# Kernel tuning notes

Measured on AMD Instinct MI355X. Metric: run time of the kernel, lower is better.

Reference implementation:

```python
import jax, jax.numpy as jnp
import numpy as np

EMB = 768

def setup_inputs() -> dict:
    key = jax.random.key(0)
    ks = jax.random.split(key, 9)
    B, N, E = 8, 2048, EMB
    s = 1.0 / np.sqrt(E)
    return {
        "x":  jax.random.normal(ks[0], (B, N, E), jnp.float32),
        "Wq": jax.random.normal(ks[1], (E, E), jnp.float32) * s,
        "bq": jnp.zeros((E,), jnp.float32),
        "Wk": jax.random.normal(ks[2], (E, E), jnp.float32) * s,
        "bk": jnp.zeros((E,), jnp.float32),
        "Wv": jax.random.normal(ks[3], (E, E), jnp.float32) * s,
        "bv": jnp.zeros((E,), jnp.float32),
        "Wo": jax.random.normal(ks[4], (E, E), jnp.float32) * s,
        "bo": jnp.zeros((E,), jnp.float32),
    }

def reference(x, Wq, bq, Wk, bk, Wv, bv, Wo, bo):
    # Single-head attention; scale uses full emb dim (as in the source).
    E = x.shape[-1]
    q = jnp.einsum('bne,ef->bnf', x, Wq) + bq
    k = jnp.einsum('bne,ef->bnf', x, Wk) + bk
    v = jnp.einsum('bne,ef->bnf', x, Wv) + bv
    scores = jnp.einsum('bqe,bke->bqk', q, k) / jnp.sqrt(jnp.asarray(E, x.dtype))
    attn = jax.nn.softmax(scores, axis=-1)  # dropout is identity in eval mode
    out = jnp.einsum('bqk,bke->bqe', attn, v)
    return jnp.einsum('bne,ef->bnf', out, Wo) + bo
```

## Files before the change

### kernel.cpp

```cpp
#include <hip/hip_runtime.h>
#include <hip/hip_fp16.h>
#include <stdint.h>

typedef unsigned short u16;
typedef __attribute__((ext_vector_type(8))) __bf16 bf16x8;
typedef __attribute__((ext_vector_type(4))) float f32x4;

#define SEQ 2048
#define EMB 768
#define NB  8
#define LDQK (2 * EMB)

#define VMCNT(n) asm volatile("s_waitcnt vmcnt(" #n ")" ::: "memory")
#define LGKM(n)                                            \
  do {                                                     \
    asm volatile("s_waitcnt lgkmcnt(" #n ")" ::: "memory"); \
    __builtin_amdgcn_sched_barrier(0);                     \
  } while (0)

__device__ __forceinline__ u16 f2bf(float f) {
  union { float f; uint32_t u; } a; a.f = f;
  uint32_t r = a.u + 0x7fffu + ((a.u >> 16) & 1u);
  return (u16)(r >> 16);
}
__device__ __forceinline__ float bf2f(u16 h) {
  union { uint32_t u; float f; } a; a.u = ((uint32_t)h) << 16;
  return a.f;
}

__device__ __forceinline__ void swz_bid(int& bx, int& by, int& bz)
{
  const int gx = gridDim.x, gy = gridDim.y;
  const int nwg = gx * gy * gridDim.z;
  const int lid = ((int)blockIdx.z * gy + (int)blockIdx.y) * gx +
                  (int)blockIdx.x;
  const int cpx = nwg >> 3;
  const int orig = (lid & 7) * cpx + (lid >> 3);
  bx = orig % gx;
  const int t = orig / gx;
  by = t % gy;
  bz = t / gy;
}

__global__ __launch_bounds__(256) void k_detect_bias(
    const u16* __restrict__ x, int* __restrict__ flag,
    const void* __restrict__ b0, const void* __restrict__ b1,
    const void* __restrict__ b2, const void* __restrict__ b3,
    float* __restrict__ biasf)
{
  const int tid = threadIdx.x;
  int bad = 0;
#pragma unroll
  for (int i = 0; i < 4; ++i) {
    const u16 h = x[(tid * 4 + i) * 2];
    const int e = (h >> 7) & 0xFF;
    bad += (e >= 160 && e <= 254) ? 1 : 0;
  }
#pragma unroll
  for (int off = 32; off > 0; off >>= 1) bad += __shfl_down(bad, off);
  __shared__ int cnt[4];
  __shared__ int sflag;
  if ((tid & 63) == 0) cnt[tid >> 6] = bad;
  __syncthreads();
  if (tid == 0) {
    const int f = (cnt[0] + cnt[1] + cnt[2] + cnt[3] > 200) ? 1 : 0;
    sflag = f;
    *flag = f;
  }
  __syncthreads();
  const int f32 = sflag;
#pragma unroll
  for (int z = 0; z < 4; ++z) {
    const void* src = (z == 0) ? b0 : (z == 1) ? b1 : (z == 2) ? b2 : b3;
#pragma unroll
    for (int i = 0; i < 3; ++i) {
      const int j = tid + i * 256;
      biasf[z * EMB + j] = f32 ? ((const float*)src)[j]
                               : bf2f(((const u16*)src)[j]);
    }
  }
}

__global__ __launch_bounds__(256) void k_convert_x(
    const void* __restrict__ src, u16* __restrict__ dst,
    const int* __restrict__ flag, int n4)
{
  const int i = blockIdx.x * 256 + threadIdx.x;
  if (i >= n4) return;
  if (*flag) {
    const float4 f = ((const float4*)src)[i];
    ushort4 o;
    o.x = f2bf(f.x); o.y = f2bf(f.y); o.z = f2bf(f.z); o.w = f2bf(f.w);
    ((ushort4*)dst)[i] = o;
  } else {
    ((ushort4*)dst)[i] = ((const ushort4*)src)[i];
  }
}

__global__ __launch_bounds__(256) void k_transpose_w(
    const void* __restrict__ W0, const void* __restrict__ W1,
    const void* __restrict__ W2, const void* __restrict__ W3,
    u16* __restrict__ WT, const int* __restrict__ flag)
{
  __shared__ u16 t[32][33];
  const int z = blockIdx.z;
  const void* in = (z == 0) ? W0 : (z == 1) ? W1 : (z == 2) ? W2 : W3;
  u16* out = WT + (size_t)z * EMB * EMB;
  const int c0 = blockIdx.x * 32, r0 = blockIdx.y * 32;
  const int tx = threadIdx.x, ty = threadIdx.y;
  const int f32 = *flag;
#pragma unroll
  for (int i = 0; i < 4; ++i) {
    const size_t idx = (size_t)(r0 + ty + i * 8) * EMB + c0 + tx;
    t[ty + i * 8][tx] = f32 ? f2bf(((const float*)in)[idx])
                            : ((const u16*)in)[idx];
  }
  __syncthreads();
#pragma unroll
  for (int i = 0; i < 4; ++i)
    out[(size_t)(c0 + ty + i * 8) * EMB + r0 + tx] = t[tx][ty + i * 8];
}

template <int EPI, int MFR, int NFR>
__device__ __forceinline__ void gemm_core256(
    const u16* __restrict__ A, int lda,
    const u16* __restrict__ BT, int ldbt,
    void* __restrict__ Cp, int ldc,
    const float* __restrict__ biasf, const int* __restrict__ of32,
    float scale, int K, int m0, int n0)
{
  constexpr int AQ = MFR * 1024;
  constexpr int BQ = NFR * 2048;
  constexpr int STRIDE = 2 * AQ + 2 * BQ;
  __shared__ __align__(16) u16 LDSU[2 * STRIDE];
  const int tid  = threadIdx.x;
  const int lane = tid & 63;
  const int wave = tid >> 6;
  const int wm   = wave >> 2;
  const int wn   = wave & 3;
  const int lrow = lane & 15;
  const int quad = lane >> 4;
  const int NT   = K >> 6;

  auto STAGEA = [&](int t, int kh) {
    constexpr int NCH = MFR * 128;
    const int buf = t & 1;
#pragma unroll
    for (int i = 0; i < 2; ++i) {
      const int c = i * 512 + tid;
      if (NCH == 1024 || c < NCH) {
        const int row = c >> 2;
        const int ss4 = (c & 3) ^ ((row >> 1) & 3);
        const u16* g = A + (size_t)(m0 + row) * lda + t * 64 + kh * 32 + ss4 * 8;
        u16* l = LDSU + buf * STRIDE + kh * AQ + (c & ~63) * 8;
        __builtin_amdgcn_global_load_lds(
            (const __attribute__((address_space(1))) void*)g,
            (__attribute__((address_space(3))) void*)l, 16, 0, 0);
      }
    }
  };
  auto STAGEB = [&](int t, int kh) {
    constexpr int NCH = NFR * 256;
    const int buf = t & 1;
#pragma unroll
    for (int i = 0; i < 2; ++i) {
      const int c = i * 512 + tid;
      if (NCH == 1024 || c < NCH) {
        const int row = c >> 2;
        const int ss4 = (c & 3) ^ ((row >> 1) & 3);
        const u16* g = BT + (size_t)(n0 + row) * ldbt + t * 64 + kh * 32 + ss4 * 8;
        u16* l = LDSU + buf * STRIDE + 2 * AQ + kh * BQ + (c & ~63) * 8;
        __builtin_amdgcn_global_load_lds(
            (const __attribute__((address_space(1))) void*)g,
            (__attribute__((address_space(3))) void*)l, 16, 0, 0);
      }
    }
  };

  auto FRAGA = [&](int t, int kh, int row) -> bf16x8 {
    const u16* p = LDSU + (t & 1) * STRIDE + kh * AQ + row * 32 +
                   ((quad ^ ((row >> 1) & 3)) * 8);
    bf16x8 r;
    asm volatile("ds_read_b128 %0, %1"
                 : "=v"(r)
                 : "v"((const __attribute__((address_space(3))) u16*)p));
    return r;
  };
  auto FRAGB = [&](int t, int kh, int row) -> bf16x8 {
    const u16* p = LDSU + (t & 1) * STRIDE + 2 * AQ + kh * BQ + row * 32 +
                   ((quad ^ ((row >> 1) & 3)) * 8);
    bf16x8 r;
    asm volatile("ds_read_b128 %0, %1"
                 : "=v"(r)
                 : "v"((const __attribute__((address_space(3))) u16*)p));
    return r;
  };

  f32x4 acc[MFR][NFR];
#pragma unroll
  for (int m = 0; m < MFR; ++m)
#pragma unroll
    for (int n = 0; n < NFR; ++n)
#pragma unroll
      for (int r = 0; r < 4; ++r) acc[m][n][r] = 0.0f;

  bf16x8 Af0[MFR], Af1[MFR], Bf0[NFR], Bf1[NFR];

  const int arow = wm * (MFR * 16) + lrow;
  const int brow = wn * (NFR * 16) + lrow;

  auto MG_LO = [&](bf16x8 (&Afr)[MFR], bf16x8 (&Bfr)[NFR]) {
#pragma unroll
    for (int m = 0; m < MFR; ++m)
#pragma unroll
      for (int n = 0; n < 2; ++n)
        acc[m][n] = __builtin_amdgcn_mfma_f32_16x16x32_bf16(
            Afr[m], Bfr[n], acc[m][n], 0, 0, 0);
  };
  auto MG_HI = [&](bf16x8 (&Afr)[MFR], bf16x8 (&Bfr)[NFR]) {
#pragma unroll
    for (int m = 0; m < MFR; ++m)
#pragma unroll
      for (int n = 2; n < NFR; ++n)
        acc[m][n] = __builtin_amdgcn_mfma_f32_16x16x32_bf16(
            Afr[m], Bfr[n], acc[m][n], 0, 0, 0);
  };

  STAGEA(0, 0); STAGEB(0, 0); STAGEA(0, 1); STAGEB(0, 1);
  STAGEA(1, 0); STAGEB(1, 0); STAGEA(1, 1); STAGEB(1, 1);
  if constexpr (MFR == 8 && NFR == 4) { VMCNT(8); } else { VMCNT(6); }
  __builtin_amdgcn_s_barrier();
#pragma unroll
  for (int m = 0; m < MFR; ++m) Af0[m] = FRAGA(0, 0, arow + m * 16);
  Bf0[0] = FRAGB(0, 0, brow);
  Bf0[1] = FRAGB(0, 0, brow + 16);

  for (int u = 0; u < NT; ++u) {
    const bool s2 = (u + 2) < NT;
#pragma unroll
    for (int n = 2; n < NFR; ++n) Bf0[n] = FRAGB(u, 0, brow + n * 16);
    if (s2) STAGEA(u + 2, 0);
    __builtin_amdgcn_s_barrier();
    if constexpr (NFR == 3) { LGKM(1); } else { LGKM(2); }
    __builtin_amdgcn_s_setprio(1);
    MG_LO(Af0, Bf0);
    __builtin_amdgcn_s_setprio(0);
    __builtin_amdgcn_s_barrier();
#pragma unroll
    for (int m = 0; m < MFR; ++m) Af1[m] = FRAGA(u, 1, arow + m * 16);
    Bf1[0] = FRAGB(u, 1, brow);
    Bf1[1] = FRAGB(u, 1, brow + 16);
    if (s2) STAGEB(u + 2, 0);
    __builtin_amdgcn_s_barrier();
    if constexpr (MFR == 6) { LGKM(8); } else { LGKM(10); }
    __builtin_amdgcn_s_setprio(1);
    MG_HI(Af0, Bf0);
    __builtin_amdgcn_s_setprio(0);
    __builtin_amdgcn_s_barrier();
#pragma unroll
    for (int n = 2; n < NFR; ++n) Bf1[n] = FRAGB(u, 1, brow + n * 16);
    if (s2) STAGEA(u + 2, 1);
    __builtin_amdgcn_s_barrier();
    if constexpr (NFR == 3) { LGKM(1); } else { LGKM(2); }
    __builtin_amdgcn_s_setprio(1);
    MG_LO(Af1, Bf1);
    __builtin_amdgcn_s_setprio(0);
    __builtin_amdgcn_s_barrier();
    if (s2) {
      if constexpr (MFR == 8 && NFR == 4)      { VMCNT(6); }
      else if constexpr (MFR == 8 && NFR == 3) { VMCNT(5); }
      else                                     { VMCNT(4); }
    } else {
      VMCNT(0);
    }
    if (s2) STAGEB(u + 2, 1);
    __builtin_amdgcn_s_barrier();
    if (u + 1 < NT) {
#pragma unroll
      for (int m = 0; m < MFR; ++m) Af0[m] = FRAGA(u + 1, 0, arow + m * 16);
      Bf0[0] = FRAGB(u + 1, 0, brow);
      Bf0[1] = FRAGB(u + 1, 0, brow + 16);
      if constexpr (MFR == 6) { LGKM(8); } else { LGKM(10); }
    } else {
      LGKM(0);
    }
    __builtin_amdgcn_s_setprio(1);
    MG_HI(Af1, Bf1);
    __builtin_amdgcn_s_setprio(0);
    __builtin_amdgcn_s_barrier();
  }

  const int rb = m0 + wm * (MFR * 16) + quad * 4;
  const int cb = n0 + wn * (NFR * 16) + lrow;
  if (EPI == 3) {
    u16* C = (u16*)Cp;
#pragma unroll
    for (int m = 0; m < MFR; ++m)
#pragma unroll
      for (int n = 0; n < NFR; ++n)
#pragma unroll
        for (int r = 0; r < 4; ++r) {
          const int row = rb + m * 16 + r;
          const int col = cb + n * 16;
          C[(size_t)row * ldc + col] =
              __half_as_ushort(__float2half(acc[m][n][r] * scale));
        }
  } else if (EPI == 2) {
    u16* C = (u16*)Cp;
#pragma unroll
    for (int m = 0; m < MFR; ++m)
#pragma unroll
      for (int n = 0; n < NFR; ++n)
#pragma unroll
        for (int r = 0; r < 4; ++r) {
          const int row = rb + m * 16 + r;
          const int col = cb + n * 16;
          C[(size_t)row * ldc + col] = f2bf(acc[m][n][r]);
        }
  } else if (EPI == 5) {
    u16* C = (u16*)Cp;
#pragma unroll
    for (int m = 0; m < MFR; ++m)
#pragma unroll
      for (int r = 0; r < 4; ++r) {
        const int row = rb + m * 16 + r;
        const float bv = biasf[row];
#pragma unroll
        for (int n = 0; n < NFR; ++n) {
          const int col = cb + n * 16;
          C[(size_t)row * ldc + col] = f2bf(acc[m][n][r] + bv);
        }
      }
  } else {
    float bv[NFR];
#pragma unroll
    for (int n = 0; n < NFR; ++n) bv[n] = biasf[cb + n * 16];
    const bool f32out = (of32 != nullptr) && (*of32 != 0);
    if (f32out) {
      float* C = (float*)Cp;
#pragma unroll
      for (int m = 0; m < MFR; ++m)
#pragma unroll
        for (int n = 0; n < NFR; ++n)
#pragma unroll
          for (int r = 0; r < 4; ++r) {
            const int row = rb + m * 16 + r;
            const int col = cb + n * 16;
            C[(size_t)row * ldc + col] = acc[m][n][r] + bv[n];
          }
    } else {
      u16* C = (u16*)Cp;
#pragma unroll
      for (int m = 0; m < MFR; ++m)
#pragma unroll
        for (int n = 0; n < NFR; ++n)
#pragma unroll
          for (int r = 0; r < 4; ++r) {
            const int row = rb + m * 16 + r;
            const int col = cb + n * 16;
            C[(size_t)row * ldc + col] = f2bf(acc[m][n][r] + bv[n]);
          }
    }
  }
}


__global__ __launch_bounds__(512) void k_gemm_qk(
    const u16* __restrict__ A, const u16* __restrict__ BT,
    u16* __restrict__ QK, const float* __restrict__ biasf)
{
  int bx, by, bz; swz_bid(bx, by, bz);
  gemm_core256<0, 8, 3>(A, EMB, BT, EMB, QK, LDQK, biasf, nullptr, 1.0f, EMB,
                        by * 256, bx * 192);
}

__global__ __launch_bounds__(512) void k_gemm_vt(
    const u16* __restrict__ WvT, const u16* __restrict__ xb,
    u16* __restrict__ VT, const float* __restrict__ biasv)
{
  int bx, by, bz; swz_bid(bx, by, bz);
  const int b = bz;
  gemm_core256<5, 6, 4>(WvT, EMB,
                        xb + (size_t)b * SEQ * EMB, EMB,
                        VT + (size_t)b * EMB * SEQ, SEQ,
                        biasv, nullptr, 1.0f, EMB,
                        by * 192, bx * 256);
}

__global__ __launch_bounds__(512) void k_gemm_out(
    const u16* __restrict__ A, const u16* __restrict__ BT,
    void* __restrict__ C, const float* __restrict__ biasf,
    const int* __restrict__ of32)
{
  int bx, by, bz; swz_bid(bx, by, bz);
  gemm_core256<0, 8, 3>(A, EMB, BT, EMB, C, EMB, biasf, of32, 1.0f, EMB,
                        by * 256, bx * 192);
}

__global__ __launch_bounds__(512) void k_gemm_scores(
    const u16* __restrict__ QK, u16* __restrict__ S, int b0)
{
  int bx, by, bz; swz_bid(bx, by, bz);
  const int b = b0 + bz;
  const u16* base = QK + (size_t)b * SEQ * LDQK;
  gemm_core256<3, 8, 4>(base, LDQK,
                        base + EMB, LDQK,
                        S + (size_t)bz * SEQ * SEQ, SEQ,
                        nullptr, nullptr,
                        0.03608439182435161f , EMB,
                        by * 256, bx * 256);
}

__global__ __launch_bounds__(512) void k_gemm_pv(
    const u16* __restrict__ P, const u16* __restrict__ VT,
    u16* __restrict__ O, int b0)
{
  int bx, by, bz; swz_bid(bx, by, bz);
  const int b = b0 + bz;
  gemm_core256<2, 8, 3>(P  + (size_t)bz * SEQ * SEQ, SEQ,
                        VT + (size_t)b * EMB * SEQ, SEQ,
                        O  + (size_t)b * SEQ * EMB, EMB,
                        nullptr, nullptr, 1.0f, SEQ,
                        by * 256, bx * 192);
}

__global__ __launch_bounds__(256) void k_softmax(u16* __restrict__ S)
{
  u16* row = S + ((size_t)blockIdx.y * SEQ + blockIdx.x) * SEQ;
  const int tid = threadIdx.x;

  uint4 raw = *(const uint4*)(row + tid * 8);
  const u16* h = (const u16*)&raw;
  float v[8];
#pragma unroll
  for (int i = 0; i < 8; ++i) v[i] = __half2float(__ushort_as_half(h[i]));

  float mx = v[0];
#pragma unroll
  for (int i = 1; i < 8; ++i) mx = fmaxf(mx, v[i]);
#pragma unroll
  for (int off = 32; off > 0; off >>= 1) mx = fmaxf(mx, __shfl_down(mx, off));
  __shared__ float red[4], red2[4];
  if ((tid & 63) == 0) red[tid >> 6] = mx;
  __syncthreads();
  mx = fmaxf(fmaxf(red[0], red[1]), fmaxf(red[2], red[3]));

  float s = 0.0f;
#pragma unroll
  for (int i = 0; i < 8; ++i) { v[i] = __expf(v[i] - mx); s += v[i]; }
#pragma unroll
  for (int off = 32; off > 0; off >>= 1) s += __shfl_down(s, off);
  if ((tid & 63) == 0) red2[tid >> 6] = s;
  __syncthreads();
  s = red2[0] + red2[1] + red2[2] + red2[3];
  const float inv = 1.0f / s;

  uint4 outv;
  u16* o = (u16*)&outv;
#pragma unroll
  for (int i = 0; i < 8; ++i) o[i] = f2bf(v[i] * inv);
  *(uint4*)(row + tid * 8) = outv;
}


extern "C" void kernel_launch(void* const* d_in, const int* in_sizes, int n_in,
                              void* d_out, int out_size, void* d_ws, size_t ws_size,
                              hipStream_t stream)
{
  (void)in_sizes; (void)n_in; (void)out_size;
  const void* x  = d_in[0];
  const void* Wq = d_in[1];
  const void* bq = d_in[2];
  const void* Wk = d_in[3];
  const void* bk = d_in[4];
  const void* Wv = d_in[5];
  const void* bv = d_in[6];
  const void* Wo = d_in[7];
  const void* bo = d_in[8];

  char* ws = (char*)d_ws;
  size_t off = 0;
  auto alloc = [&](size_t bytes) -> void* {
    void* p = ws + off;
    off += (bytes + 255) & ~(size_t)255;
    return p;
  };
  int*   flag  = (int*)alloc(256);
  u16*   xb    = (u16*)alloc((size_t)NB * SEQ * EMB * 2);
  u16*   QK    = (u16*)alloc((size_t)NB * SEQ * LDQK * 2);
  u16*   VT    = (u16*)alloc((size_t)NB * EMB * SEQ * 2);
  u16*   O     = (u16*)alloc((size_t)NB * SEQ * EMB * 2);
  u16*   WT    = (u16*)alloc((size_t)4 * EMB * EMB * 2);
  float* biasf = (float*)alloc((size_t)4 * EMB * 4);
  u16*   S     = (u16*)(ws + off);
  size_t rem   = (ws_size > off) ? ws_size - off : 0;

  int GB = 8;
  while (GB > 1 && (size_t)GB * ((size_t)SEQ * SEQ * 2) > rem) GB >>= 1;

  k_detect_bias<<<1, 256, 0, stream>>>((const u16*)x, flag, bq, bk, bv, bo,
                                       biasf);
  const int n4 = NB * SEQ * EMB / 4;
  k_convert_x<<<(n4 + 255) / 256, 256, 0, stream>>>(x, xb, flag, n4);
  k_transpose_w<<<dim3(EMB / 32, EMB / 32, 4), dim3(32, 8), 0, stream>>>(
      Wq, Wk, Wv, Wo, WT, flag);

  k_gemm_qk<<<dim3(8, 64), 512, 0, stream>>>(xb, WT, QK, biasf);
  k_gemm_vt<<<dim3(8, 4, NB), 512, 0, stream>>>(
      WT + (size_t)2 * EMB * EMB, xb, VT, biasf + 2 * EMB);

  for (int g = 0; g < NB; g += GB) {
    k_gemm_scores<<<dim3(8, 8, GB), 512, 0, stream>>>(QK, S, g);
    k_softmax<<<dim3(SEQ, GB), 256, 0, stream>>>(S);
    k_gemm_pv<<<dim3(4, 8, GB), 512, 0, stream>>>(S, VT, O, g);
  }

  k_gemm_out<<<dim3(4, 64), 512, 0, stream>>>(O, WT + 3 * EMB * EMB, d_out,
                                              biasf + 3 * EMB, flag);
}
```

Before: 347.3 us.

## Restructure GEMM main loop into two full-K-half phases per iteration

Replaces the four-phase LO/HI split of MFMA groups with two phases per K tile, each issuing all MFMAs for one K half while the fragment reads for the other half and the global stages are in flight. This halves the number of barriers per iteration and makes MFMA bursts longer. In exchange, more LDS reads are outstanding at once (higher register pressure), the staging of both A and B is batched, and the lgkm/vmcnt wait counts were recomputed, which could be wrong if the counts do not match the issued loads.

```diff
diff --git a/kernel.cpp b/kernel.cpp
--- a/kernel.cpp
+++ b/kernel.cpp
@@ -209,83 +209,56 @@
   const int arow = wm * (MFR * 16) + lrow;
   const int brow = wn * (NFR * 16) + lrow;
 
-  auto MG_LO = [&](bf16x8 (&Afr)[MFR], bf16x8 (&Bfr)[NFR]) {
+  auto READK = [&](int t, int kh, bf16x8 (&Af)[MFR], bf16x8 (&Bf)[NFR]) {
+#pragma unroll
+    for (int m = 0; m < MFR; ++m) Af[m] = FRAGA(t, kh, arow + m * 16);
+#pragma unroll
+    for (int n = 0; n < NFR; ++n) Bf[n] = FRAGB(t, kh, brow + n * 16);
+  };
+  auto MFMA_ALL = [&](bf16x8 (&Af)[MFR], bf16x8 (&Bf)[NFR]) {
 #pragma unroll
     for (int m = 0; m < MFR; ++m)
 #pragma unroll
-      for (int n = 0; n < 2; ++n)
+      for (int n = 0; n < NFR; ++n)
         acc[m][n] = __builtin_amdgcn_mfma_f32_16x16x32_bf16(
-            Afr[m], Bfr[n], acc[m][n], 0, 0, 0);
-  };
-  auto MG_HI = [&](bf16x8 (&Afr)[MFR], bf16x8 (&Bfr)[NFR]) {
-#pragma unroll
-    for (int m = 0; m < MFR; ++m)
-#pragma unroll
-      for (int n = 2; n < NFR; ++n)
-        acc[m][n] = __builtin_amdgcn_mfma_f32_16x16x32_bf16(
-            Afr[m], Bfr[n], acc[m][n], 0, 0, 0);
+            Af[m], Bf[n], acc[m][n], 0, 0, 0);
   };
 
   STAGEA(0, 0); STAGEB(0, 0); STAGEA(0, 1); STAGEB(0, 1);
   STAGEA(1, 0); STAGEB(1, 0); STAGEA(1, 1); STAGEB(1, 1);
   if constexpr (MFR == 8 && NFR == 4) { VMCNT(8); } else { VMCNT(6); }
   __builtin_amdgcn_s_barrier();
-#pragma unroll
-  for (int m = 0; m < MFR; ++m) Af0[m] = FRAGA(0, 0, arow + m * 16);
-  Bf0[0] = FRAGB(0, 0, brow);
-  Bf0[1] = FRAGB(0, 0, brow + 16);
+  READK(0, 0, Af0, Bf0);
 
   for (int u = 0; u < NT; ++u) {
     const bool s2 = (u + 2) < NT;
-#pragma unroll
-    for (int n = 2; n < NFR; ++n) Bf0[n] = FRAGB(u, 0, brow + n * 16);
-    if (s2) STAGEA(u + 2, 0);
+    READK(u, 1, Af1, Bf1);
+    if (s2) { STAGEA(u + 2, 0); STAGEB(u + 2, 0); }
     __builtin_amdgcn_s_barrier();
-    if constexpr (NFR == 3) { LGKM(1); } else { LGKM(2); }
+    if constexpr (MFR + NFR == 12)      { LGKM(12); }
+    else if constexpr (MFR + NFR == 11) { LGKM(11); }
+    else                                { LGKM(10); }
     __builtin_amdgcn_s_setprio(1);
-    MG_LO(Af0, Bf0);
-    __builtin_amdgcn_s_setprio(0);
-    __builtin_amdgcn_s_barrier();
-#pragma unroll
-    for (int m = 0; m < MFR; ++m) Af1[m] = FRAGA(u, 1, arow + m * 16);
-    Bf1[0] = FRAGB(u, 1, brow);
-    Bf1[1] = FRAGB(u, 1, brow + 16);
-    if (s2) STAGEB(u + 2, 0);
-    __builtin_amdgcn_s_barrier();
-    if constexpr (MFR == 6) { LGKM(8); } else { LGKM(10); }
-    __builtin_amdgcn_s_setprio(1);
-    MG_HI(Af0, Bf0);
-    __builtin_amdgcn_s_setprio(0);
-    __builtin_amdgcn_s_barrier();
-#pragma unroll
-    for (int n = 2; n < NFR; ++n) Bf1[n] = FRAGB(u, 1, brow + n * 16);
-    if (s2) STAGEA(u + 2, 1);
-    __builtin_amdgcn_s_barrier();
-    if constexpr (NFR == 3) { LGKM(1); } else { LGKM(2); }
-    __builtin_amdgcn_s_setprio(1);
-    MG_LO(Af1, Bf1);
+    MFMA_ALL(Af0, Bf0);
     __builtin_amdgcn_s_setprio(0);
     __builtin_amdgcn_s_barrier();
     if (s2) {
-      if constexpr (MFR == 8 && NFR == 4)      { VMCNT(6); }
-      else if constexpr (MFR == 8 && NFR == 3) { VMCNT(5); }
-      else                                     { VMCNT(4); }
+      STAGEA(u + 2, 1); STAGEB(u + 2, 1);
+      if constexpr (MFR == 8 && NFR == 4) { VMCNT(8); } else { VMCNT(6); }
     } else {
       VMCNT(0);
     }
-    if (s2) STAGEB(u + 2, 1);
     __builtin_amdgcn_s_barrier();
     if (u + 1 < NT) {
-#pragma unroll
-      for (int m = 0; m < MFR; ++m) Af0[m] = FRAGA(u + 1, 0, arow + m * 16);
-      Bf0[0] = FRAGB(u + 1, 0, brow);
-      Bf0[1] = FRAGB(u + 1, 0, brow + 16);
-      if constexpr (MFR == 6) { LGKM(8); } else { LGKM(10); }
+      READK(u + 1, 0, Af0, Bf0);
+      if constexpr (MFR + NFR == 12)      { LGKM(12); }
+      else if constexpr (MFR + NFR == 11) { LGKM(11); }
+      else                                { LGKM(10); }
     } else {
       LGKM(0);
     }
     __builtin_amdgcn_s_setprio(1);
-    MG_HI(Af1, Bf1);
+    MFMA_ALL(Af1, Bf1);
     __builtin_amdgcn_s_setprio(0);
     __builtin_amdgcn_s_barrier();
   }
```

Result: slower. 368.2 us (+6.0%).
